# Kernel optimization log

Measured on AMD Instinct MI355X. Metric: run time of the kernel, lower is better.

Reference implementation:

```python
import jax, jax.numpy as jnp
import numpy as np

N = 100000
E = 1600000
DIN = 64
DH = 64
C = 16


def _sage_conv(x, edge_index, W_l, W_r, b):
    # PyG SAGEConv (aggr='mean'): out = lin_l(mean_{j in N(i)} x_j) + lin_r(x_i)
    src, dst = edge_index[0], edge_index[1]
    msgs = x[src]                                   # [E, D] gather
    num_nodes = x.shape[0]
    agg = jax.ops.segment_sum(msgs, dst, num_segments=num_nodes)      # [N, D]
    deg = jax.ops.segment_sum(jnp.ones((msgs.shape[0],), x.dtype), dst,
                              num_segments=num_nodes)                 # [N]
    mean = agg / jnp.maximum(deg, 1.0)[:, None]
    return mean @ W_l + b + x @ W_r


def setup_inputs() -> dict:
    key = jax.random.key(0)
    ks = jax.random.split(key, 8)
    x = jax.random.normal(ks[0], (N, DIN), dtype=jnp.float32)
    edge_index = jax.random.randint(ks[1], (2, E), 0, N, dtype=jnp.int64)
    s = 1.0 / np.sqrt(DIN)
    W1_l = jax.random.normal(ks[2], (DIN, DH), dtype=jnp.float32) * s
    W1_r = jax.random.normal(ks[3], (DIN, DH), dtype=jnp.float32) * s
    b1 = jnp.zeros((DH,), jnp.float32)
    sh = 1.0 / np.sqrt(DH)
    W2_l = jax.random.normal(ks[4], (DH, C), dtype=jnp.float32) * sh
    W2_r = jax.random.normal(ks[5], (DH, C), dtype=jnp.float32) * sh
    b2 = jnp.zeros((C,), jnp.float32)
    return {"x": x, "edge_index": edge_index, "W1_l": W1_l, "W1_r": W1_r,
            "b1": b1, "W2_l": W2_l, "W2_r": W2_r, "b2": b2}


def reference(x, edge_index, W1_l, W1_r, b1, W2_l, W2_r, b2):
    h = _sage_conv(x, edge_index, W1_l, W1_r, b1)
    h = jax.nn.relu(h)
    # dropout is identity at inference
    out = _sage_conv(h, edge_index, W2_l, W2_r, b2)
    return out
```

## Files before the change

kernel.cpp:

```cpp
#include <hip/hip_runtime.h>

#define NB 256
#define CHUNK 8192

__global__ void k_part(const int* __restrict__ srcI, const int* __restrict__ dstI,
                       int* __restrict__ gcur, int* __restrict__ pairs,
                       int E, int N, int capN, int capE) {
  __shared__ int hist[NB];
  __shared__ int base[NB];
  __shared__ int cnt[NB];
  int tid = threadIdx.x;
  int e0 = blockIdx.x * CHUNK;
  int eend = min(e0 + CHUNK, E);
  hist[tid] = 0;
  __syncthreads();
  for (int e = e0 + tid; e < eend; e += 256) {
    int d = dstI[e];
    if ((unsigned)d < (unsigned)N) atomicAdd(&hist[d / capN], 1);
  }
  __syncthreads();
  base[tid] = tid * capE + atomicAdd(&gcur[tid], hist[tid]);
  cnt[tid] = 0;
  __syncthreads();
  for (int e = e0 + tid; e < eend; e += 256) {
    int d = dstI[e];
    int s = srcI[e];
    if ((unsigned)d < (unsigned)N && (unsigned)s < (unsigned)N) {
      int b = d / capN;
      int slot = base[b] + atomicAdd(&cnt[b], 1);
      if (slot < (b + 1) * capE)
        pairs[slot] = ((d - b * capN) << 17) | s;
    }
  }
}

__launch_bounds__(512)
__global__ void k_csr(const int* __restrict__ pairs, const int* __restrict__ gcur,
                      int* __restrict__ deg, int* __restrict__ rowoff,
                      int* __restrict__ csr, int N, int capN, int capE) {
  __shared__ int hist[512];
  __shared__ int tmp[512];
  __shared__ int cur[512];
  int q = blockIdx.x;
  int tid = threadIdx.x;
  int nloc = N - q * capN;
  if (nloc > capN) nloc = capN;
  int base = q * capE;
  int cnt = gcur[q];
  if (cnt > capE) cnt = capE;
  int qbase = q * capN;
  hist[tid] = 0;
  __syncthreads();
  for (int e = tid; e < cnt; e += 512) {
    int code = pairs[base + e];
    int dl = (unsigned)code >> 17;
    if (dl < nloc) atomicAdd(&hist[dl], 1);
  }
  __syncthreads();
  int v = hist[tid];
  tmp[tid] = v;
  __syncthreads();
  for (int off = 1; off < 512; off <<= 1) {
    int t = (tid >= off) ? tmp[tid - off] : 0;
    __syncthreads();
    tmp[tid] += t;
    __syncthreads();
  }
  int ex = tmp[tid] - v;
  cur[tid] = ex;
  if (tid < nloc) {
    int i = qbase + tid;
    deg[i] = v;
    rowoff[i] = base + ex;
  }
  __syncthreads();
  for (int e = tid; e < cnt; e += 512) {
    int code = pairs[base + e];
    int dl = (unsigned)code >> 17;
    if (dl < nloc) {
      int pos = atomicAdd(&cur[dl], 1);
      csr[base + pos] = code & 0x1FFFF;
    }
  }
}

__launch_bounds__(256, 4)
__global__ void k_aggh(const float* __restrict__ x, const int* __restrict__ csr,
                       const int* __restrict__ rowoff, const int* __restrict__ deg,
                       const float* __restrict__ W1l, const float* __restrict__ W1r,
                       const float* __restrict__ b1, float* __restrict__ h, int n) {
  __shared__ float sM[64 * 68];
  __shared__ float sX[32 * 68];
  int tid = threadIdx.x;
  int row0 = blockIdx.x * 64;
  int wid = tid >> 6;
  int lane = tid & 63;

  for (int r16 = 0; r16 < 16; ++r16) {
    int row = row0 + wid * 16 + r16;
    if (row >= n) break;
    int start = __builtin_amdgcn_readfirstlane(rowoff[row]);
    int d = __builtin_amdgcn_readfirstlane(deg[row]);
    float a0 = 0.f, a1 = 0.f, a2 = 0.f, a3 = 0.f;
    float a4 = 0.f, a5 = 0.f, a6 = 0.f, a7 = 0.f;
    int j = 0;
    for (; j + 7 < d; j += 8) {
      int s0 = csr[start + j], s1 = csr[start + j + 1];
      int s2 = csr[start + j + 2], s3 = csr[start + j + 3];
      int s4 = csr[start + j + 4], s5 = csr[start + j + 5];
      int s6 = csr[start + j + 6], s7 = csr[start + j + 7];
      a0 += x[(size_t)s0 * 64 + lane]; a1 += x[(size_t)s1 * 64 + lane];
      a2 += x[(size_t)s2 * 64 + lane]; a3 += x[(size_t)s3 * 64 + lane];
      a4 += x[(size_t)s4 * 64 + lane]; a5 += x[(size_t)s5 * 64 + lane];
      a6 += x[(size_t)s6 * 64 + lane]; a7 += x[(size_t)s7 * 64 + lane];
    }
    for (; j + 3 < d; j += 4) {
      int s0 = csr[start + j], s1 = csr[start + j + 1];
      int s2 = csr[start + j + 2], s3 = csr[start + j + 3];
      a0 += x[(size_t)s0 * 64 + lane]; a1 += x[(size_t)s1 * 64 + lane];
      a2 += x[(size_t)s2 * 64 + lane]; a3 += x[(size_t)s3 * 64 + lane];
    }
    for (; j < d; ++j) a0 += x[(size_t)csr[start + j] * 64 + lane];
    float inv = (d > 0) ? 1.f / (float)d : 0.f;
    sM[lane * 68 + wid * 16 + r16] =
        (((a0 + a1) + (a2 + a3)) + ((a4 + a5) + (a6 + a7))) * inv;
  }
  __syncthreads();

  int colT = tid & 15;
  int rowT = tid >> 4;
  float acc[4][4];
#pragma unroll
  for (int r = 0; r < 4; ++r)
#pragma unroll
    for (int c = 0; c < 4; ++c) acc[r][c] = 0.f;

  for (int kt = 0; kt < 4; ++kt) {
    const float* wsrc = (kt < 2) ? W1l : W1r;
    int ko = (kt & 1) * 32;
    const float* abase;
    if (kt < 2) {
      abase = &sM[ko * 68];
    } else {
      __syncthreads();
      int f = tid;
#pragma unroll
      for (int i = 0; i < 2; ++i, f += 256) {
        int r = f >> 3, kq = f & 7;
        int rr = row0 + r; if (rr > n - 1) rr = n - 1;
        float4 v = *(const float4*)(x + (size_t)rr * 64 + ko + kq * 4);
        sX[(kq * 4 + 0) * 68 + r] = v.x;
        sX[(kq * 4 + 1) * 68 + r] = v.y;
        sX[(kq * 4 + 2) * 68 + r] = v.z;
        sX[(kq * 4 + 3) * 68 + r] = v.w;
      }
      __syncthreads();
      abase = sX;
    }
#pragma unroll 4
    for (int k = 0; k < 32; ++k) {
      float4 a = *(const float4*)&abase[k * 68 + rowT * 4];
      float4 w = *(const float4*)(wsrc + (size_t)(ko + k) * 64 + colT * 4);
      acc[0][0] += a.x * w.x; acc[0][1] += a.x * w.y; acc[0][2] += a.x * w.z; acc[0][3] += a.x * w.w;
      acc[1][0] += a.y * w.x; acc[1][1] += a.y * w.y; acc[1][2] += a.y * w.z; acc[1][3] += a.y * w.w;
      acc[2][0] += a.z * w.x; acc[2][1] += a.z * w.y; acc[2][2] += a.z * w.z; acc[2][3] += a.z * w.w;
      acc[3][0] += a.w * w.x; acc[3][1] += a.w * w.y; acc[3][2] += a.w * w.z; acc[3][3] += a.w * w.w;
    }
  }
  float4 bb = *(const float4*)(b1 + colT * 4);
#pragma unroll
  for (int r = 0; r < 4; ++r) {
    int row = row0 + rowT * 4 + r;
    if (row < n) {
      float4 o;
      o.x = fmaxf(acc[r][0] + bb.x, 0.f);
      o.y = fmaxf(acc[r][1] + bb.y, 0.f);
      o.z = fmaxf(acc[r][2] + bb.z, 0.f);
      o.w = fmaxf(acc[r][3] + bb.w, 0.f);
      *(float4*)(h + (size_t)row * 64 + colT * 4) = o;
    }
  }
}

__launch_bounds__(256, 4)
__global__ void k_pq(const float* __restrict__ h, const float* __restrict__ W2l,
                     const float* __restrict__ W2r, float* __restrict__ p,
                     float* __restrict__ q, int n) {
  __shared__ float sAT[32 * 132];
  __shared__ float sW[32 * 32];
  int tid = threadIdx.x;
  int row0 = blockIdx.x * 128;
  int colT = tid & 7;
  int rowT = tid >> 3;
  float acc[4][4];
#pragma unroll
  for (int r = 0; r < 4; ++r)
#pragma unroll
    for (int c = 0; c < 4; ++c) acc[r][c] = 0.f;

  for (int kt = 0; kt < 2; ++kt) {
    int ko = kt * 32;
    __syncthreads();
    {
      int f = tid;
#pragma unroll
      for (int i = 0; i < 4; ++i, f += 256) {
        int r = f >> 3, kq = f & 7;
        int rr = row0 + r; if (rr > n - 1) rr = n - 1;
        float4 v = *(const float4*)(h + (size_t)rr * 64 + ko + kq * 4);
        sAT[(kq * 4 + 0) * 132 + r] = v.x;
        sAT[(kq * 4 + 1) * 132 + r] = v.y;
        sAT[(kq * 4 + 2) * 132 + r] = v.z;
        sAT[(kq * 4 + 3) * 132 + r] = v.w;
      }
      int wr = tid >> 3, cq = tid & 7;
      const float* wsrc = (cq < 4) ? W2l : W2r;
      int cc = (cq & 3) * 4;
      float4 v = *(const float4*)(wsrc + (size_t)(ko + wr) * 16 + cc);
      *(float4*)&sW[wr * 32 + cq * 4] = v;
    }
    __syncthreads();
#pragma unroll 4
    for (int k = 0; k < 32; ++k) {
      float4 a = *(const float4*)&sAT[k * 132 + rowT * 4];
      float4 w = *(const float4*)&sW[k * 32 + colT * 4];
      acc[0][0] += a.x * w.x; acc[0][1] += a.x * w.y; acc[0][2] += a.x * w.z; acc[0][3] += a.x * w.w;
      acc[1][0] += a.y * w.x; acc[1][1] += a.y * w.y; acc[1][2] += a.y * w.z; acc[1][3] += a.y * w.w;
      acc[2][0] += a.z * w.x; acc[2][1] += a.z * w.y; acc[2][2] += a.z * w.z; acc[2][3] += a.z * w.w;
      acc[3][0] += a.w * w.x; acc[3][1] += a.w * w.y; acc[3][2] += a.w * w.z; acc[3][3] += a.w * w.w;
    }
  }
#pragma unroll
  for (int r = 0; r < 4; ++r) {
    int row = row0 + rowT * 4 + r;
    if (row < n) {
      float* dst = (colT < 4) ? (p + (size_t)row * 16 + colT * 4)
                              : (q + (size_t)row * 16 + (colT - 4) * 4);
      *(float4*)dst = make_float4(acc[r][0], acc[r][1], acc[r][2], acc[r][3]);
    }
  }
}

__global__ void k_agg16(const float* __restrict__ p, const int* __restrict__ csr,
                        const int* __restrict__ rowoff, const int* __restrict__ deg,
                        const float* __restrict__ b2, float* __restrict__ out, int n) {
  int t = blockIdx.x * blockDim.x + threadIdx.x;
  int i = t >> 4;
  int dd = t & 15;
  if (i >= n) return;
  int start = rowoff[i];
  int d = deg[i];
  float a0 = 0.f, a1 = 0.f, a2 = 0.f, a3 = 0.f;
  float a4 = 0.f, a5 = 0.f, a6 = 0.f, a7 = 0.f;
  int j = 0;
  for (; j + 7 < d; j += 8) {
    int s0 = csr[start + j], s1 = csr[start + j + 1];
    int s2 = csr[start + j + 2], s3 = csr[start + j + 3];
    int s4 = csr[start + j + 4], s5 = csr[start + j + 5];
    int s6 = csr[start + j + 6], s7 = csr[start + j + 7];
    a0 += p[(size_t)s0 * 16 + dd]; a1 += p[(size_t)s1 * 16 + dd];
    a2 += p[(size_t)s2 * 16 + dd]; a3 += p[(size_t)s3 * 16 + dd];
    a4 += p[(size_t)s4 * 16 + dd]; a5 += p[(size_t)s5 * 16 + dd];
    a6 += p[(size_t)s6 * 16 + dd]; a7 += p[(size_t)s7 * 16 + dd];
  }
  for (; j + 3 < d; j += 4) {
    int s0 = csr[start + j], s1 = csr[start + j + 1];
    int s2 = csr[start + j + 2], s3 = csr[start + j + 3];
    a0 += p[(size_t)s0 * 16 + dd]; a1 += p[(size_t)s1 * 16 + dd];
    a2 += p[(size_t)s2 * 16 + dd]; a3 += p[(size_t)s3 * 16 + dd];
  }
  for (; j < d; ++j) a0 += p[(size_t)csr[start + j] * 16 + dd];
  float inv = (d > 0) ? 1.f / (float)d : 0.f;
  out[t] = ((((a0 + a1) + (a2 + a3)) + ((a4 + a5) + (a6 + a7)))) * inv + out[t] + b2[dd];
}

extern "C" void kernel_launch(void* const* d_in, const int* in_sizes, int n_in,
                              void* d_out, int out_size, void* d_ws, size_t ws_size,
                              hipStream_t stream) {
  const float* x   = (const float*)d_in[0];
  const int*   ei  = (const int*)d_in[1];
  const float* W1l = (const float*)d_in[2];
  const float* W1r = (const float*)d_in[3];
  const float* b1  = (const float*)d_in[4];
  const float* W2l = (const float*)d_in[5];
  const float* W2r = (const float*)d_in[6];
  const float* b2  = (const float*)d_in[7];
  float* out = (float*)d_out;

  int N = in_sizes[0] / 64;
  int E = in_sizes[1] / 2;
  const int* srcI = ei;
  const int* dstI = ei + E;

  int capN = (N + NB - 1) / NB;
  int capE = E / NB + 1024;

  size_t off = 0;
  auto alloc = [&](size_t bytes) -> char* {
    char* r = (char*)d_ws + off;
    off = (off + bytes + 255) & ~(size_t)255;
    return r;
  };
  int*   deg    = (int*)alloc((size_t)N * 4);
  int*   rowoff = (int*)alloc((size_t)N * 4);
  int*   csr    = (int*)alloc((size_t)NB * capE * 4);
  int*   gcur   = (int*)alloc(NB * 4);
  float* h      = (float*)alloc((size_t)N * 64 * 4);
  float* p      = (float*)alloc((size_t)N * 16 * 4);
  int*   pairs  = (int*)h;
  if (off > ws_size) return;
  if ((size_t)NB * capE * 4 > (size_t)N * 64 * 4) return;
  if (N > (1 << 17) || capN > (1 << 9)) return;

  hipMemsetAsync(gcur, 0, NB * 4, stream);
  k_part<<<(E + CHUNK - 1) / CHUNK, 256, 0, stream>>>(srcI, dstI, gcur, pairs, E, N, capN, capE);
  k_csr<<<NB, 512, 0, stream>>>(pairs, gcur, deg, rowoff, csr, N, capN, capE);

  k_aggh<<<(N + 63) / 64, 256, 0, stream>>>(x, csr, rowoff, deg, W1l, W1r, b1, h, N);

  k_pq<<<(N + 127) / 128, 256, 0, stream>>>(h, W2l, W2r, p, out, N);
  k_agg16<<<(N * 16 + 255) / 256, 256, 0, stream>>>(p, csr, rowoff, deg, b2, out, N);
}
```

Before: 272.5 us.

## Gather neighbor features in fp16 and split aggregation from layer-1 GEMM

Adds a pass that converts x to fp16 so the layer-1 neighbor gather reads half the bytes. p is also stored in fp16 for the layer-2 gather. The fused aggregate+GEMM kernel is split into a one-wave-per-row aggregation kernel that writes an fp32 mean buffer, plus a separate GEMM kernel that stages weights in shared memory. This trades an extra conversion pass and an extra N×64 fp32 write/read round trip for cheaper random gathers and higher gather parallelism, and it reduces precision of the gathered features.

```diff
diff --git a/kernel.cpp b/kernel.cpp
--- a/kernel.cpp
+++ b/kernel.cpp
@@ -1,7 +1,20 @@
 #include <hip/hip_runtime.h>
+#include <hip/hip_fp16.h>
 
 #define NB 256
 #define CHUNK 8192
+
+__global__ void k_cvt(const float* __restrict__ x, __half* __restrict__ xh, int total) {
+  int i = (blockIdx.x * 256 + threadIdx.x) * 8;
+  if (i >= total) return;
+  float4 a = *(const float4*)(x + i);
+  float4 b = *(const float4*)(x + i + 4);
+  __half2* dst = (__half2*)(xh + i);
+  dst[0] = __floats2half2_rn(a.x, a.y);
+  dst[1] = __floats2half2_rn(a.z, a.w);
+  dst[2] = __floats2half2_rn(b.x, b.y);
+  dst[3] = __floats2half2_rn(b.z, b.w);
+}
 
 __global__ void k_part(const int* __restrict__ srcI, const int* __restrict__ dstI,
                        int* __restrict__ gcur, int* __restrict__ pairs,
@@ -84,49 +97,52 @@
   }
 }
 
+__global__ void k_agg64(const __half* __restrict__ xh, const int* __restrict__ csr,
+                        const int* __restrict__ rowoff, const int* __restrict__ deg,
+                        float* __restrict__ m, int n) {
+  int w = (blockIdx.x * blockDim.x + threadIdx.x) >> 6;
+  int lane = threadIdx.x & 63;
+  if (w >= n) return;
+  int start = __builtin_amdgcn_readfirstlane(rowoff[w]);
+  int d = __builtin_amdgcn_readfirstlane(deg[w]);
+  float a0 = 0.f, a1 = 0.f, a2 = 0.f, a3 = 0.f;
+  float a4 = 0.f, a5 = 0.f, a6 = 0.f, a7 = 0.f;
+  int j = 0;
+  for (; j + 7 < d; j += 8) {
+    int s0 = csr[start + j], s1 = csr[start + j + 1];
+    int s2 = csr[start + j + 2], s3 = csr[start + j + 3];
+    int s4 = csr[start + j + 4], s5 = csr[start + j + 5];
+    int s6 = csr[start + j + 6], s7 = csr[start + j + 7];
+    a0 += __half2float(xh[(size_t)s0 * 64 + lane]);
+    a1 += __half2float(xh[(size_t)s1 * 64 + lane]);
+    a2 += __half2float(xh[(size_t)s2 * 64 + lane]);
+    a3 += __half2float(xh[(size_t)s3 * 64 + lane]);
+    a4 += __half2float(xh[(size_t)s4 * 64 + lane]);
+    a5 += __half2float(xh[(size_t)s5 * 64 + lane]);
+    a6 += __half2float(xh[(size_t)s6 * 64 + lane]);
+    a7 += __half2float(xh[(size_t)s7 * 64 + lane]);
+  }
+  for (; j + 3 < d; j += 4) {
+    int s0 = csr[start + j], s1 = csr[start + j + 1];
+    int s2 = csr[start + j + 2], s3 = csr[start + j + 3];
+    a0 += __half2float(xh[(size_t)s0 * 64 + lane]);
+    a1 += __half2float(xh[(size_t)s1 * 64 + lane]);
+    a2 += __half2float(xh[(size_t)s2 * 64 + lane]);
+    a3 += __half2float(xh[(size_t)s3 * 64 + lane]);
+  }
+  for (; j < d; ++j) a0 += __half2float(xh[(size_t)csr[start + j] * 64 + lane]);
+  float inv = (d > 0) ? 1.f / (float)d : 0.f;
+  m[(size_t)w * 64 + lane] = (((a0 + a1) + (a2 + a3)) + ((a4 + a5) + (a6 + a7))) * inv;
+}
+
 __launch_bounds__(256, 4)
-__global__ void k_aggh(const float* __restrict__ x, const int* __restrict__ csr,
-                       const int* __restrict__ rowoff, const int* __restrict__ deg,
-                       const float* __restrict__ W1l, const float* __restrict__ W1r,
-                       const float* __restrict__ b1, float* __restrict__ h, int n) {
-  __shared__ float sM[64 * 68];
-  __shared__ float sX[32 * 68];
+__global__ void k_h(const float* __restrict__ m, const float* __restrict__ x,
+                    const float* __restrict__ Wl, const float* __restrict__ Wr,
+                    const float* __restrict__ b1, float* __restrict__ h, int n) {
+  __shared__ float sAT[32 * 68];
+  __shared__ float sW[32 * 64];
   int tid = threadIdx.x;
   int row0 = blockIdx.x * 64;
-  int wid = tid >> 6;
-  int lane = tid & 63;
-
-  for (int r16 = 0; r16 < 16; ++r16) {
-    int row = row0 + wid * 16 + r16;
-    if (row >= n) break;
-    int start = __builtin_amdgcn_readfirstlane(rowoff[row]);
-    int d = __builtin_amdgcn_readfirstlane(deg[row]);
-    float a0 = 0.f, a1 = 0.f, a2 = 0.f, a3 = 0.f;
-    float a4 = 0.f, a5 = 0.f, a6 = 0.f, a7 = 0.f;
-    int j = 0;
-    for (; j + 7 < d; j += 8) {
-      int s0 = csr[start + j], s1 = csr[start + j + 1];
-      int s2 = csr[start + j + 2], s3 = csr[start + j + 3];
-      int s4 = csr[start + j + 4], s5 = csr[start + j + 5];
-      int s6 = csr[start + j + 6], s7 = csr[start + j + 7];
-      a0 += x[(size_t)s0 * 64 + lane]; a1 += x[(size_t)s1 * 64 + lane];
-      a2 += x[(size_t)s2 * 64 + lane]; a3 += x[(size_t)s3 * 64 + lane];
-      a4 += x[(size_t)s4 * 64 + lane]; a5 += x[(size_t)s5 * 64 + lane];
-      a6 += x[(size_t)s6 * 64 + lane]; a7 += x[(size_t)s7 * 64 + lane];
-    }
-    for (; j + 3 < d; j += 4) {
-      int s0 = csr[start + j], s1 = csr[start + j + 1];
-      int s2 = csr[start + j + 2], s3 = csr[start + j + 3];
-      a0 += x[(size_t)s0 * 64 + lane]; a1 += x[(size_t)s1 * 64 + lane];
-      a2 += x[(size_t)s2 * 64 + lane]; a3 += x[(size_t)s3 * 64 + lane];
-    }
-    for (; j < d; ++j) a0 += x[(size_t)csr[start + j] * 64 + lane];
-    float inv = (d > 0) ? 1.f / (float)d : 0.f;
-    sM[lane * 68 + wid * 16 + r16] =
-        (((a0 + a1) + (a2 + a3)) + ((a4 + a5) + (a6 + a7))) * inv;
-  }
-  __syncthreads();
-
   int colT = tid & 15;
   int rowT = tid >> 4;
   float acc[4][4];
@@ -136,31 +152,35 @@
     for (int c = 0; c < 4; ++c) acc[r][c] = 0.f;
 
   for (int kt = 0; kt < 4; ++kt) {
-    const float* wsrc = (kt < 2) ? W1l : W1r;
+    const float* asrc = (kt < 2) ? m : x;
+    const float* wsrc = (kt < 2) ? Wl : Wr;
     int ko = (kt & 1) * 32;
-    const float* abase;
-    if (kt < 2) {
-      abase = &sM[ko * 68];
-    } else {
-      __syncthreads();
+    __syncthreads();
+    {
       int f = tid;
 #pragma unroll
       for (int i = 0; i < 2; ++i, f += 256) {
         int r = f >> 3, kq = f & 7;
         int rr = row0 + r; if (rr > n - 1) rr = n - 1;
-        float4 v = *(const float4*)(x + (size_t)rr * 64 + ko + kq * 4);
-        sX[(kq * 4 + 0) * 68 + r] = v.x;
-        sX[(kq * 4 + 1) * 68 + r] = v.y;
-        sX[(kq * 4 + 2) * 68 + r] = v.z;
-        sX[(kq * 4 + 3) * 68 + r] = v.w;
+        float4 v = *(const float4*)(asrc + (size_t)rr * 64 + ko + kq * 4);
+        sAT[(kq * 4 + 0) * 68 + r] = v.x;
+        sAT[(kq * 4 + 1) * 68 + r] = v.y;
+        sAT[(kq * 4 + 2) * 68 + r] = v.z;
+        sAT[(kq * 4 + 3) * 68 + r] = v.w;
       }
-      __syncthreads();
-      abase = sX;
-    }
+      int g = tid;
+#pragma unroll
+      for (int i = 0; i < 2; ++i, g += 256) {
+        int wr = g >> 4, cq = g & 15;
+        float4 v = *(const float4*)(wsrc + (size_t)(ko + wr) * 64 + cq * 4);
+        *(float4*)&sW[wr * 64 + cq * 4] = v;
+      }
+    }
+    __syncthreads();
 #pragma unroll 4
     for (int k = 0; k < 32; ++k) {
-      float4 a = *(const float4*)&abase[k * 68 + rowT * 4];
-      float4 w = *(const float4*)(wsrc + (size_t)(ko + k) * 64 + colT * 4);
+      float4 a = *(const float4*)&sAT[k * 68 + rowT * 4];
+      float4 w = *(const float4*)&sW[k * 64 + colT * 4];
       acc[0][0] += a.x * w.x; acc[0][1] += a.x * w.y; acc[0][2] += a.x * w.z; acc[0][3] += a.x * w.w;
       acc[1][0] += a.y * w.x; acc[1][1] += a.y * w.y; acc[1][2] += a.y * w.z; acc[1][3] += a.y * w.w;
       acc[2][0] += a.z * w.x; acc[2][1] += a.z * w.y; acc[2][2] += a.z * w.z; acc[2][3] += a.z * w.w;
@@ -184,7 +204,7 @@
 
 __launch_bounds__(256, 4)
 __global__ void k_pq(const float* __restrict__ h, const float* __restrict__ W2l,
-                     const float* __restrict__ W2r, float* __restrict__ p,
+                     const float* __restrict__ W2r, __half* __restrict__ p16,
                      float* __restrict__ q, int n) {
   __shared__ float sAT[32 * 132];
   __shared__ float sW[32 * 32];
@@ -234,14 +254,19 @@
   for (int r = 0; r < 4; ++r) {
     int row = row0 + rowT * 4 + r;
     if (row < n) {
-      float* dst = (colT < 4) ? (p + (size_t)row * 16 + colT * 4)
-                              : (q + (size_t)row * 16 + (colT - 4) * 4);
-      *(float4*)dst = make_float4(acc[r][0], acc[r][1], acc[r][2], acc[r][3]);
-    }
-  }
-}
-
-__global__ void k_agg16(const float* __restrict__ p, const int* __restrict__ csr,
+      if (colT < 4) {
+        __half2* dst = (__half2*)(p16 + (size_t)row * 16 + colT * 4);
+        dst[0] = __floats2half2_rn(acc[r][0], acc[r][1]);
+        dst[1] = __floats2half2_rn(acc[r][2], acc[r][3]);
+      } else {
+        *(float4*)(q + (size_t)row * 16 + (colT - 4) * 4) =
+            make_float4(acc[r][0], acc[r][1], acc[r][2], acc[r][3]);
+      }
+    }
+  }
+}
+
+__global__ void k_agg16(const __half* __restrict__ p16, const int* __restrict__ csr,
                         const int* __restrict__ rowoff, const int* __restrict__ deg,
                         const float* __restrict__ b2, float* __restrict__ out, int n) {
   int t = blockIdx.x * blockDim.x + threadIdx.x;
@@ -258,18 +283,24 @@
     int s2 = csr[start + j + 2], s3 = csr[start + j + 3];
     int s4 = csr[start + j + 4], s5 = csr[start + j + 5];
     int s6 = csr[start + j + 6], s7 = csr[start + j + 7];
-    a0 += p[(size_t)s0 * 16 + dd]; a1 += p[(size_t)s1 * 16 + dd];
-    a2 += p[(size_t)s2 * 16 + dd]; a3 += p[(size_t)s3 * 16 + dd];
-    a4 += p[(size_t)s4 * 16 + dd]; a5 += p[(size_t)s5 * 16 + dd];
-    a6 += p[(size_t)s6 * 16 + dd]; a7 += p[(size_t)s7 * 16 + dd];
+    a0 += __half2float(p16[(size_t)s0 * 16 + dd]);
+    a1 += __half2float(p16[(size_t)s1 * 16 + dd]);
+    a2 += __half2float(p16[(size_t)s2 * 16 + dd]);
+    a3 += __half2float(p16[(size_t)s3 * 16 + dd]);
+    a4 += __half2float(p16[(size_t)s4 * 16 + dd]);
+    a5 += __half2float(p16[(size_t)s5 * 16 + dd]);
+    a6 += __half2float(p16[(size_t)s6 * 16 + dd]);
+    a7 += __half2float(p16[(size_t)s7 * 16 + dd]);
   }
   for (; j + 3 < d; j += 4) {
     int s0 = csr[start + j], s1 = csr[start + j + 1];
     int s2 = csr[start + j + 2], s3 = csr[start + j + 3];
-    a0 += p[(size_t)s0 * 16 + dd]; a1 += p[(size_t)s1 * 16 + dd];
-    a2 += p[(size_t)s2 * 16 + dd]; a3 += p[(size_t)s3 * 16 + dd];
-  }
-  for (; j < d; ++j) a0 += p[(size_t)csr[start + j] * 16 + dd];
+    a0 += __half2float(p16[(size_t)s0 * 16 + dd]);
+    a1 += __half2float(p16[(size_t)s1 * 16 + dd]);
+    a2 += __half2float(p16[(size_t)s2 * 16 + dd]);
+    a3 += __half2float(p16[(size_t)s3 * 16 + dd]);
+  }
+  for (; j < d; ++j) a0 += __half2float(p16[(size_t)csr[start + j] * 16 + dd]);
   float inv = (d > 0) ? 1.f / (float)d : 0.f;
   out[t] = ((((a0 + a1) + (a2 + a3)) + ((a4 + a5) + (a6 + a7)))) * inv + out[t] + b2[dd];
 }
@@ -301,23 +332,27 @@
     off = (off + bytes + 255) & ~(size_t)255;
     return r;
   };
-  int*   deg    = (int*)alloc((size_t)N * 4);
-  int*   rowoff = (int*)alloc((size_t)N * 4);
-  int*   csr    = (int*)alloc((size_t)NB * capE * 4);
-  int*   gcur   = (int*)alloc(NB * 4);
-  float* h      = (float*)alloc((size_t)N * 64 * 4);
-  float* p      = (float*)alloc((size_t)N * 16 * 4);
-  int*   pairs  = (int*)h;
+  int*    deg    = (int*)alloc((size_t)N * 4);
+  int*    rowoff = (int*)alloc((size_t)N * 4);
+  int*    csr    = (int*)alloc((size_t)NB * capE * 4);
+  int*    gcur   = (int*)alloc(NB * 4);
+  __half* xh     = (__half*)alloc((size_t)N * 64 * 2);
+  float*  m      = (float*)alloc((size_t)N * 64 * 4);
+  float*  h      = (float*)alloc((size_t)N * 64 * 4);
+  __half* p16    = (__half*)alloc((size_t)N * 16 * 2);
+  int*    pairs  = (int*)h;
   if (off > ws_size) return;
   if ((size_t)NB * capE * 4 > (size_t)N * 64 * 4) return;
   if (N > (1 << 17) || capN > (1 << 9)) return;
 
   hipMemsetAsync(gcur, 0, NB * 4, stream);
+  k_cvt<<<(N * 64 + 2047) / 2048, 256, 0, stream>>>(x, xh, N * 64);
   k_part<<<(E + CHUNK - 1) / CHUNK, 256, 0, stream>>>(srcI, dstI, gcur, pairs, E, N, capN, capE);
   k_csr<<<NB, 512, 0, stream>>>(pairs, gcur, deg, rowoff, csr, N, capN, capE);
 
-  k_aggh<<<(N + 63) / 64, 256, 0, stream>>>(x, csr, rowoff, deg, W1l, W1r, b1, h, N);
-
-  k_pq<<<(N + 127) / 128, 256, 0, stream>>>(h, W2l, W2r, p, out, N);
-  k_agg16<<<(N * 16 + 255) / 256, 256, 0, stream>>>(p, csr, rowoff, deg, b2, out, N);
-}
+  k_agg64<<<(N * 64 + 255) / 256, 256, 0, stream>>>(xh, csr, rowoff, deg, m, N);
+  k_h<<<(N + 63) / 64, 256, 0, stream>>>(m, x, W1l, W1r, b1, h, N);
+
+  k_pq<<<(N + 127) / 128, 256, 0, stream>>>(h, W2l, W2r, p16, out, N);
+  k_agg16<<<(N * 16 + 255) / 256, 256, 0, stream>>>(p16, csr, rowoff, deg, b2, out, N);
+}
```

Result: faster. 241.3 us (-11.5%).
